# Optimization experiments

Measured on AMD Instinct MI355X. Metric: run time of the kernel, lower is better.

Reference implementation:

```python
import jax, jax.numpy as jnp
import numpy as np

B, N, D = 8, 1024, 256
H, DK, DV = 8, 64, 64
NEG = -1.0e9


def setup_inputs() -> dict:
    key = jax.random.key(0)
    ks = jax.random.split(key, 8)
    node_features = jax.random.normal(ks[0], (B, N, D), dtype=jnp.float32)
    em = (jax.random.uniform(ks[1], (B, 1, N, N)) < 0.03).astype(jnp.float32)
    eye = jnp.eye(N, dtype=jnp.float32)[None, None]
    edge_mask = jnp.maximum(em, eye)
    distance_weights = jax.random.uniform(ks[2], (B, N), dtype=jnp.float32)
    s = 1.0 / np.sqrt(D)
    Wq = jax.random.normal(ks[3], (D, H * DK), dtype=jnp.float32) * s
    Wk = jax.random.normal(ks[4], (D, H * DK), dtype=jnp.float32) * s
    Wv = jax.random.normal(ks[5], (D, H * DV), dtype=jnp.float32) * s
    Wo = jax.random.normal(ks[6], (H * DV, D), dtype=jnp.float32) / np.sqrt(H * DV)
    bo = jnp.zeros((D,), dtype=jnp.float32)
    return {"node_features": node_features, "edge_mask": edge_mask,
            "distance_weights": distance_weights,
            "Wq": Wq, "Wk": Wk, "Wv": Wv, "Wo": Wo, "bo": bo}


def reference(node_features, edge_mask, distance_weights, Wq, Wk, Wv, Wo, bo):
    b, n, d = node_features.shape
    # project and split heads: [B, H, N, dk]
    q = (node_features @ Wq).reshape(b, n, H, DK).transpose(0, 2, 1, 3)
    k = (node_features @ Wk).reshape(b, n, H, DK).transpose(0, 2, 1, 3)
    v = (node_features @ Wv).reshape(b, n, H, DV).transpose(0, 2, 1, 3)
    # scaled dot-product logits [B, H, N, N]
    logits = jnp.einsum('bhsd,bhtd->bhst', q, k) / jnp.sqrt(jnp.float32(DK))
    # additive edge-mask bias (masked pairs pushed to -1e9)
    logits = logits + (1.0 - edge_mask) * NEG
    # multiplicative per-key distance modulation
    logits = logits * distance_weights[:, None, None, :]
    w = jax.nn.softmax(logits, axis=-1)
    out = jnp.einsum('bhst,bhtd->bhsd', w, v)
    out = out.transpose(0, 2, 1, 3).reshape(b, n, H * DV)
    return out @ Wo + bo
```

## Files before the change

kernel.cpp:

```cpp
#include <hip/hip_runtime.h>
#include <hip/hip_bf16.h>
#include <hip/hip_fp16.h>
#include <cstdint>

#define B_ 8
#define N_ 1024
#define D_ 256
#define H_ 8
#define HD_ 512

typedef _Float16 f16;
typedef _Float16 f16x8 __attribute__((ext_vector_type(8)));
typedef _Float16 f16x4 __attribute__((ext_vector_type(4)));
typedef float f32x4 __attribute__((ext_vector_type(4)));
typedef unsigned long long ull;
typedef unsigned long long ull2 __attribute__((ext_vector_type(2)));

__device__ __forceinline__ void gload16(const void* g, void* l) {
    __builtin_amdgcn_global_load_lds(
        (const __attribute__((address_space(1))) unsigned int*)(uintptr_t)g,
        (__attribute__((address_space(3))) unsigned int*)(uintptr_t)l,
        16, 0, 0);
}

template<int RN>
__device__ __forceinline__ float rowror(float x) {
    return __builtin_bit_cast(float, __builtin_amdgcn_mov_dpp(
        __builtin_bit_cast(int, x), 0x120 + RN, 0xf, 0xf, true));
}
__device__ __forceinline__ float rowmax16(float x) {
    x = fmaxf(x, rowror<1>(x)); x = fmaxf(x, rowror<2>(x));
    x = fmaxf(x, rowror<4>(x)); x = fmaxf(x, rowror<8>(x));
    return x;
}
__device__ __forceinline__ float rowsum16(float x) {
    x += rowror<1>(x); x += rowror<2>(x);
    x += rowror<4>(x); x += rowror<8>(x);
    return x;
}

__global__ __launch_bounds__(256) void pack_mask_kernel(
    const float* __restrict__ mask, ull* __restrict__ bmT)
{
    const int wv = threadIdx.x >> 6, lane = threadIdx.x & 63;
    const int r = blockIdx.x * 4 + wv;
    const int b = r >> 10, n = r & 1023;
    const float* row = mask + ((size_t)b * N_ + n) * N_;
    for (int tt = 0; tt < 16; ++tt) {
        float v = row[tt * 64 + lane];
        ull m = __ballot(v != 0.0f);
        if (lane == 0) bmT[((size_t)b * 16 + tt) * N_ + n] = m;
    }
}

__global__ __launch_bounds__(256) void wconv_qkv_kernel(
    const float* __restrict__ Wq, const float* __restrict__ Wk,
    const float* __restrict__ Wv, f16* __restrict__ WT)
{
    __shared__ float Ws[64][65];
    const int tid = threadIdx.x;
    const int c0 = blockIdx.x * 64, k0 = blockIdx.y * 64;
    const int m = c0 >> 9, cw0 = c0 & 511;
    const float* Wsel = (m == 0) ? Wq : (m == 1) ? Wk : Wv;
    const float scale = (m == 0) ? 0.125f : 1.0f;
    const int rr = tid >> 6, cc = tid & 63;
    for (int i = 0; i < 16; ++i)
        Ws[i * 4 + rr][cc] = Wsel[(size_t)(k0 + i * 4 + rr) * HD_ + cw0 + cc];
    __syncthreads();
    for (int i = 0; i < 16; ++i)
        WT[(size_t)(c0 + i * 4 + rr) * D_ + k0 + cc] = (f16)(Ws[cc][i * 4 + rr] * scale);
}

__global__ __launch_bounds__(256) void wconv_o_kernel(
    const float* __restrict__ Wo, f16* __restrict__ WToT)
{
    __shared__ float Ws[64][65];
    const int tid = threadIdx.x;
    const int c0 = blockIdx.x * 64, k0 = blockIdx.y * 64;
    const int rr = tid >> 6, cc = tid & 63;
    for (int i = 0; i < 16; ++i)
        Ws[i * 4 + rr][cc] = Wo[(size_t)(k0 + i * 4 + rr) * D_ + c0 + cc];
    __syncthreads();
    for (int i = 0; i < 16; ++i)
        WToT[(size_t)(c0 + i * 4 + rr) * HD_ + k0 + cc] = (f16)Ws[cc][i * 4 + rr];
}

__global__ __launch_bounds__(256) void xconv_kernel(
    const float* __restrict__ X, f16* __restrict__ Xh)
{
    const size_t i = (size_t)(blockIdx.x * 256 + threadIdx.x) * 4;
    f32x4 v = *reinterpret_cast<const f32x4*>(X + i);
    f16x4 h;
    for (int j = 0; j < 4; ++j) h[j] = (f16)v[j];
    *reinterpret_cast<f16x4*>(Xh + i) = h;
}

__global__ __launch_bounds__(256, 4) void qkv_kernel(
    const f16* __restrict__ Xh, const f16* __restrict__ WT,
    f16* __restrict__ Qh, f16* __restrict__ Kh, f16* __restrict__ Vt)
{
    __shared__ f16 Wsh[2][8192];
    const int tid = threadIdx.x;
    const int wv = tid >> 6, lane = tid & 63;
    const int g = lane >> 4, li = lane & 15;
    const int row0 = blockIdx.x * 64;
    const int c0 = blockIdx.y * 128;
    const int m = c0 >> 9, cw0 = c0 & 511;

    f32x4 acc[4][2] = {};

    auto stage = [&](int ks, int bf) {
        for (int i = 0; i < 4; ++i) {
            const int idx = i * 256 + tid;
            const int c = idx >> 3, ch = idx & 7;
            const f16* src = WT + (size_t)(c0 + c) * D_ + ks * 64 + ((ch ^ (c & 7)) * 8);
            gload16(src, &Wsh[bf][idx * 8]);
        }
    };
    stage(0, 0);
    __syncthreads();
    int bf = 0;
    for (int ks = 0; ks < 4; ++ks) {
        if (ks < 3) stage(ks + 1, bf ^ 1);
        for (int kk = 0; kk < 2; ++kk) {
            f16x8 af[4];
            for (int rf = 0; rf < 4; ++rf)
                af[rf] = *reinterpret_cast<const f16x8*>(
                    Xh + (size_t)(row0 + rf * 16 + li) * D_ + ks * 64 + kk * 32 + g * 8);
            for (int cf = 0; cf < 2; ++cf) {
                const int cl = wv * 32 + cf * 16 + li;
                f16x8 bm_ = *reinterpret_cast<const f16x8*>(
                    &Wsh[bf][cl * 64 + (((kk * 4 + g) ^ (cl & 7)) * 8)]);
                for (int rf = 0; rf < 4; ++rf)
                    acc[rf][cf] = __builtin_amdgcn_mfma_f32_16x16x32_f16(
                        af[rf], bm_, acc[rf][cf], 0, 0, 0);
            }
        }
        __syncthreads();
        bf ^= 1;
    }
    const int b = row0 >> 10;
    for (int cf = 0; cf < 2; ++cf) {
        const int cw = cw0 + wv * 32 + cf * 16 + li;
        const int h = cw >> 6, dk = cw & 63;
        for (int rf = 0; rf < 4; ++rf) {
            const int nloc = (row0 & 1023) + rf * 16 + g * 4;
            if (m < 2) {
                f16* dst = (m == 0 ? Qh : Kh) + ((size_t)(b * H_ + h) * N_ + nloc) * 64 + dk;
                for (int j = 0; j < 4; ++j) dst[(size_t)j * 64] = (f16)acc[rf][cf][j];
            } else {
                f16x4 v4;
                for (int j = 0; j < 4; ++j) v4[j] = (f16)acc[rf][cf][j];
                *reinterpret_cast<f16x4*>(
                    Vt + ((size_t)(b * H_ + h) * 64 + dk) * N_ + nloc) = v4;
            }
        }
    }
}

__global__ __launch_bounds__(256, 4) void attn_kernel(
    const f16* __restrict__ Qh, const f16* __restrict__ Kh,
    const f16* __restrict__ Vt,
    const ull* __restrict__ bm, const float* __restrict__ dw,
    f16* __restrict__ AO)
{
    __shared__ f16 Ksh[8192];
    __shared__ f16 Vsh[8192];
    __shared__ f16 Ps[4096];
    const int tid = threadIdx.x;
    const int wv = tid >> 6, lane = tid & 63;
    const int g = lane >> 4, li = lane & 15;
    const int bid = (blockIdx.x & 7) * 128 + (blockIdx.x >> 3);
    const int st = bid & 15, h = (bid >> 4) & 7, b = bid >> 7;
    const int s0 = st * 64 + wv * 16;

    const f16* Qbase = Qh + (size_t)(b * H_ + h) * N_ * 64;
    const f16* Kbase = Kh + (size_t)(b * H_ + h) * N_ * 64;
    const f16* Vbase = Vt + (size_t)(b * H_ + h) * 64 * N_;

    f16x8 qf0 = *reinterpret_cast<const f16x8*>(Qbase + (size_t)(s0 + li) * 64 + g * 8);
    f16x8 qf1 = *reinterpret_cast<const f16x8*>(Qbase + (size_t)(s0 + li) * 64 + 32 + g * 8);

    int ro0[4], ro1[4];
    for (int fc = 0; fc < 4; ++fc) {
        const int r = fc * 16 + li;
        ro0[fc] = r * 64 + ((g ^ (r & 7)) * 8);
        ro1[fc] = r * 64 + (((4 | g) ^ (r & 7)) * 8);
    }
    const int pr0 = wv * 1024 + li * 64 + ((g ^ (li & 7)) * 8);
    const int pr1 = wv * 1024 + li * 64 + (((4 | g) ^ (li & 7)) * 8);

    const int s0i = wv * 64 + lane, s1i = 256 + wv * 64 + lane;
    const int r0_ = s0i >> 3, c0_ = ((s0i & 7) ^ (r0_ & 7)) * 8;
    const int r1_ = s1i >> 3, c1_ = ((s1i & 7) ^ (r1_ & 7)) * 8;
    const f16* kp0 = Kbase + r0_ * 64 + c0_;
    const f16* kp1 = Kbase + r1_ * 64 + c1_;
    const f16* vp0 = Vbase + (size_t)r0_ * N_ + c0_;
    const f16* vp1 = Vbase + (size_t)r1_ * N_ + c1_;
    f16* const kd0 = Ksh + s0i * 8;
    f16* const kd1 = Ksh + s1i * 8;
    f16* const vd0 = Vsh + s0i * 8;
    f16* const vd1 = Vsh + s1i * 8;

    const ull* bmp = bm + (size_t)b * 16 * N_ + s0 + g * 4;
    const float* dwp = dw + b * N_ + li;

    f32x4 of[4] = {};
    float m_run[4], l_run[4];
    for (int j = 0; j < 4; ++j) { m_run[j] = -1e30f; l_run[j] = 0.f; }

    gload16(kp0, kd0); gload16(kp1, kd1);
    gload16(vp0, vd0); gload16(vp1, vd1);
    kp0 += 4096; kp1 += 4096; vp0 += 64; vp1 += 64;
    __syncthreads();
    int koff = 0;

    for (int tt = 0; tt < 16; ++tt) {
        if (tt < 15) {
            const int nb = koff ^ 4096;
            gload16(kp0, kd0 + nb); gload16(kp1, kd1 + nb);
            gload16(vp0, vd0 + nb); gload16(vp1, vd1 + nb);
            kp0 += 4096; kp1 += 4096; vp0 += 64; vp1 += 64;
        }
        ull2 w01 = *reinterpret_cast<const ull2*>(bmp);
        ull2 w23 = *reinterpret_cast<const ull2*>(bmp + 2);
        bmp += N_;
        float dwc[4], bdw[4];
        for (int fc = 0; fc < 4; ++fc) {
            dwc[fc] = dwp[fc * 16] * 1.442695041f;
            bdw[fc] = dwc[fc] * -1.0e9f;
        }
        dwp += 64;

        f32x4 s[4] = {};
        for (int fc = 0; fc < 4; ++fc) {
            f16x8 kf0 = *reinterpret_cast<const f16x8*>(Ksh + koff + ro0[fc]);
            f16x8 kf1 = *reinterpret_cast<const f16x8*>(Ksh + koff + ro1[fc]);
            s[fc] = __builtin_amdgcn_mfma_f32_16x16x32_f16(qf0, kf0, s[fc], 0, 0, 0);
            s[fc] = __builtin_amdgcn_mfma_f32_16x16x32_f16(qf1, kf1, s[fc], 0, 0, 0);
        }
        ull wsh[4];
        wsh[0] = w01.x >> li; wsh[1] = w01.y >> li;
        wsh[2] = w23.x >> li; wsh[3] = w23.y >> li;

        float mt[4] = {-1e30f, -1e30f, -1e30f, -1e30f};
        for (int fc = 0; fc < 4; ++fc)
            for (int j = 0; j < 4; ++j) {
                const float sel = ((wsh[j] >> (fc * 16)) & 1ull) ? 0.0f : bdw[fc];
                const float lg = fmaf(s[fc][j], dwc[fc], sel);
                s[fc][j] = lg;
                mt[j] = fmaxf(mt[j], lg);
            }
        float alpha[4];
        for (int j = 0; j < 4; ++j) {
            mt[j] = rowmax16(mt[j]);
            const float mn = fmaxf(m_run[j], mt[j]);
            alpha[j] = __builtin_amdgcn_exp2f(m_run[j] - mn);
            m_run[j] = mn;
        }
        float rs[4] = {0.f, 0.f, 0.f, 0.f};
        for (int fc = 0; fc < 4; ++fc)
            for (int j = 0; j < 4; ++j) {
                const float p = __builtin_amdgcn_exp2f(s[fc][j] - m_run[j]);
                s[fc][j] = p;
                rs[j] += p;
            }
        for (int j = 0; j < 4; ++j) {
            rs[j] = rowsum16(rs[j]);
            l_run[j] = l_run[j] * alpha[j] + rs[j];
        }
        for (int fc = 0; fc < 4; ++fc)
            for (int j = 0; j < 4; ++j) of[fc][j] *= alpha[j];

        {
            f16* psw = Ps + wv * 1024;
            for (int fc = 0; fc < 4; ++fc)
                for (int j = 0; j < 4; ++j) {
                    const int r = g * 4 + j;
                    psw[r * 64 + (((fc * 2 + (li >> 3)) ^ (r & 7)) * 8) + (li & 7)]
                        = (f16)s[fc][j];
                }
            f16x8 pf0 = *reinterpret_cast<const f16x8*>(Ps + pr0);
            f16x8 pf1 = *reinterpret_cast<const f16x8*>(Ps + pr1);
            for (int fc = 0; fc < 4; ++fc) {
                f16x8 vf0 = *reinterpret_cast<const f16x8*>(Vsh + koff + ro0[fc]);
                f16x8 vf1 = *reinterpret_cast<const f16x8*>(Vsh + koff + ro1[fc]);
                of[fc] = __builtin_amdgcn_mfma_f32_16x16x32_f16(pf0, vf0, of[fc], 0, 0, 0);
                of[fc] = __builtin_amdgcn_mfma_f32_16x16x32_f16(pf1, vf1, of[fc], 0, 0, 0);
            }
        }
        __syncthreads();
        koff ^= 4096;
    }
    for (int j = 0; j < 4; ++j) {
        const float inv = 1.f / l_run[j];
        const int srow = s0 + g * 4 + j;
        f16* dst = AO + ((size_t)b * N_ + srow) * HD_ + h * 64;
        for (int fc = 0; fc < 4; ++fc)
            dst[fc * 16 + li] = (f16)(of[fc][j] * inv);
    }
}

__global__ __launch_bounds__(256, 4) void proj_kernel(
    const f16* __restrict__ AO, const f16* __restrict__ WToT,
    const float* __restrict__ bo, float* __restrict__ out)
{
    __shared__ f16 Ash[16 * 512];
    const int tid = threadIdx.x;
    const int wv = tid >> 6, lane = tid & 63;
    const int g = lane >> 4, li = lane & 15;
    const int row0 = blockIdx.x * 16;
    const int c0 = wv * 64;

    for (int i = 0; i < 4; ++i) {
        const int idx = i * 256 + tid;
        const int r = idx >> 6, ch = idx & 63;
        const f16* src = AO + (size_t)(row0 + r) * HD_ + ((ch ^ (r & 7)) * 8);
        gload16(src, &Ash[idx * 8]);
    }
    __syncthreads();

    f32x4 acc[4] = {};
    for (int k0 = 0; k0 < HD_; k0 += 32) {
        const int cb = k0 >> 3;
        f16x8 af = *reinterpret_cast<const f16x8*>(
            &Ash[li * HD_ + (((cb + g) ^ (li & 7)) * 8)]);
        for (int fc = 0; fc < 4; ++fc) {
            f16x8 bf = *reinterpret_cast<const f16x8*>(
                WToT + (size_t)(c0 + fc * 16 + li) * HD_ + k0 + g * 8);
            acc[fc] = __builtin_amdgcn_mfma_f32_16x16x32_f16(af, bf, acc[fc], 0, 0, 0);
        }
    }
    for (int fc = 0; fc < 4; ++fc) {
        const int c = c0 + fc * 16 + li;
        const float bias = bo[c];
        for (int j = 0; j < 4; ++j)
            out[(size_t)(row0 + g * 4 + j) * D_ + c] = acc[fc][j] + bias;
    }
}

extern "C" void kernel_launch(void* const* d_in, const int* in_sizes, int n_in,
                              void* d_out, int out_size, void* d_ws, size_t ws_size,
                              hipStream_t stream) {
    const float* X    = (const float*)d_in[0];
    const float* mask = (const float*)d_in[1];
    const float* dwv  = (const float*)d_in[2];
    const float* Wq   = (const float*)d_in[3];
    const float* Wk   = (const float*)d_in[4];
    const float* Wv   = (const float*)d_in[5];
    const float* Wo   = (const float*)d_in[6];
    const float* bo   = (const float*)d_in[7];
    float* out = (float*)d_out;

    const size_t per = (size_t)B_ * H_ * N_ * 64;
    f16* Qh = (f16*)d_ws;
    f16* Kh = Qh + per;
    f16* Vt = Kh + per;
    f16* AO = Vt + per;
    f16* WToT = (f16*)d_ws;

    ull* bmT   = (ull*)d_out;
    f16* WTqkv = (f16*)((char*)d_out + (1u << 20));
    f16* Xh    = (f16*)((char*)d_out + (2u << 20));

    pack_mask_kernel<<<dim3(2048), 256, 0, stream>>>(mask, bmT);
    wconv_qkv_kernel<<<dim3(24, 4), 256, 0, stream>>>(Wq, Wk, Wv, WTqkv);
    xconv_kernel<<<dim3(2048), 256, 0, stream>>>(X, Xh);
    qkv_kernel<<<dim3(128, 12), 256, 0, stream>>>(Xh, WTqkv, Qh, Kh, Vt);
    attn_kernel<<<dim3(1024), 256, 0, stream>>>(Qh, Kh, Vt, bmT, dwv, AO);
    wconv_o_kernel<<<dim3(4, 8), 256, 0, stream>>>(Wo, WToT);
    proj_kernel<<<dim3(512, 1), 256, 0, stream>>>(AO, WToT, bo, out);
}
```

Before: 198.7 us.

## Merge preprocessing kernels, stage X in LDS, lazy softmax rescale, MFMA priority

Three preprocessing launches (mask bit-packing, QKV weight transpose, X fp16 conversion) become one kernel that dispatches on block index, removing two launches. The QKV GEMM now stages X tiles into swizzled LDS with async global-to-LDS loads instead of reading fragments straight from global memory, and its occupancy hint drops from 4 to 3. The attention kernel skips the online-softmax rescale of the accumulator and running sum unless some row's max grows by more than 8 in log2 units. s_setprio brackets are added around MFMA sections. The lazy rescale lets exponentials exceed 1 and trades a wave-wide vote for skipped multiplies.

```diff
diff --git a/kernel.cpp b/kernel.cpp
--- a/kernel.cpp
+++ b/kernel.cpp
@@ -39,36 +39,45 @@
     return x;
 }
 
-__global__ __launch_bounds__(256) void pack_mask_kernel(
-    const float* __restrict__ mask, ull* __restrict__ bmT)
-{
-    const int wv = threadIdx.x >> 6, lane = threadIdx.x & 63;
-    const int r = blockIdx.x * 4 + wv;
-    const int b = r >> 10, n = r & 1023;
-    const float* row = mask + ((size_t)b * N_ + n) * N_;
-    for (int tt = 0; tt < 16; ++tt) {
-        float v = row[tt * 64 + lane];
-        ull m = __ballot(v != 0.0f);
-        if (lane == 0) bmT[((size_t)b * 16 + tt) * N_ + n] = m;
-    }
-}
-
-__global__ __launch_bounds__(256) void wconv_qkv_kernel(
+__global__ __launch_bounds__(256) void pre_kernel(
+    const float* __restrict__ mask, ull* __restrict__ bmT,
     const float* __restrict__ Wq, const float* __restrict__ Wk,
-    const float* __restrict__ Wv, f16* __restrict__ WT)
+    const float* __restrict__ Wv, f16* __restrict__ WT,
+    const float* __restrict__ X, f16* __restrict__ Xh)
 {
     __shared__ float Ws[64][65];
-    const int tid = threadIdx.x;
-    const int c0 = blockIdx.x * 64, k0 = blockIdx.y * 64;
-    const int m = c0 >> 9, cw0 = c0 & 511;
-    const float* Wsel = (m == 0) ? Wq : (m == 1) ? Wk : Wv;
-    const float scale = (m == 0) ? 0.125f : 1.0f;
-    const int rr = tid >> 6, cc = tid & 63;
-    for (int i = 0; i < 16; ++i)
-        Ws[i * 4 + rr][cc] = Wsel[(size_t)(k0 + i * 4 + rr) * HD_ + cw0 + cc];
-    __syncthreads();
-    for (int i = 0; i < 16; ++i)
-        WT[(size_t)(c0 + i * 4 + rr) * D_ + k0 + cc] = (f16)(Ws[cc][i * 4 + rr] * scale);
+    const int bid = blockIdx.x;
+    const int tid = threadIdx.x;
+    if (bid < 2048) {
+        const int wv = tid >> 6, lane = tid & 63;
+        const int r = bid * 4 + wv;
+        const int b = r >> 10, n = r & 1023;
+        const float* row = mask + ((size_t)b * N_ + n) * N_;
+        for (int tt = 0; tt < 16; ++tt) {
+            float v = row[tt * 64 + lane];
+            ull m = __ballot(v != 0.0f);
+            if (lane == 0) bmT[((size_t)b * 16 + tt) * N_ + n] = m;
+        }
+    } else if (bid < 2144) {
+        const int t = bid - 2048;
+        const int c0 = (t % 24) * 64, k0 = (t / 24) * 64;
+        const int m = c0 >> 9, cw0 = c0 & 511;
+        const float* Wsel = (m == 0) ? Wq : (m == 1) ? Wk : Wv;
+        const float scale = (m == 0) ? 0.125f : 1.0f;
+        const int rr = tid >> 6, cc = tid & 63;
+        for (int i = 0; i < 16; ++i)
+            Ws[i * 4 + rr][cc] = Wsel[(size_t)(k0 + i * 4 + rr) * HD_ + cw0 + cc];
+        __syncthreads();
+        for (int i = 0; i < 16; ++i)
+            WT[(size_t)(c0 + i * 4 + rr) * D_ + k0 + cc] =
+                (f16)(Ws[cc][i * 4 + rr] * scale);
+    } else {
+        const size_t i = (size_t)((bid - 2144) * 256 + tid) * 4;
+        f32x4 v = *reinterpret_cast<const f32x4*>(X + i);
+        f16x4 h2;
+        for (int j = 0; j < 4; ++j) h2[j] = (f16)v[j];
+        *reinterpret_cast<f16x4*>(Xh + i) = h2;
+    }
 }
 
 __global__ __launch_bounds__(256) void wconv_o_kernel(
@@ -85,20 +94,11 @@
         WToT[(size_t)(c0 + i * 4 + rr) * HD_ + k0 + cc] = (f16)Ws[cc][i * 4 + rr];
 }
 
-__global__ __launch_bounds__(256) void xconv_kernel(
-    const float* __restrict__ X, f16* __restrict__ Xh)
-{
-    const size_t i = (size_t)(blockIdx.x * 256 + threadIdx.x) * 4;
-    f32x4 v = *reinterpret_cast<const f32x4*>(X + i);
-    f16x4 h;
-    for (int j = 0; j < 4; ++j) h[j] = (f16)v[j];
-    *reinterpret_cast<f16x4*>(Xh + i) = h;
-}
-
-__global__ __launch_bounds__(256, 4) void qkv_kernel(
+__global__ __launch_bounds__(256, 3) void qkv_kernel(
     const f16* __restrict__ Xh, const f16* __restrict__ WT,
     f16* __restrict__ Qh, f16* __restrict__ Kh, f16* __restrict__ Vt)
 {
+    __shared__ f16 Ash[2][4096];
     __shared__ f16 Wsh[2][8192];
     const int tid = threadIdx.x;
     const int wv = tid >> 6, lane = tid & 63;
@@ -110,6 +110,12 @@
     f32x4 acc[4][2] = {};
 
     auto stage = [&](int ks, int bf) {
+        for (int i = 0; i < 2; ++i) {
+            const int idx = i * 256 + tid;
+            const int r = idx >> 3, ch = idx & 7;
+            const f16* src = Xh + (size_t)(row0 + r) * D_ + ks * 64 + ((ch ^ (r & 7)) * 8);
+            gload16(src, &Ash[bf][idx * 8]);
+        }
         for (int i = 0; i < 4; ++i) {
             const int idx = i * 256 + tid;
             const int c = idx >> 3, ch = idx & 7;
@@ -124,9 +130,12 @@
         if (ks < 3) stage(ks + 1, bf ^ 1);
         for (int kk = 0; kk < 2; ++kk) {
             f16x8 af[4];
-            for (int rf = 0; rf < 4; ++rf)
+            for (int rf = 0; rf < 4; ++rf) {
+                const int r = rf * 16 + li;
                 af[rf] = *reinterpret_cast<const f16x8*>(
-                    Xh + (size_t)(row0 + rf * 16 + li) * D_ + ks * 64 + kk * 32 + g * 8);
+                    &Ash[bf][r * 64 + (((kk * 4 + g) ^ (r & 7)) * 8)]);
+            }
+            __builtin_amdgcn_s_setprio(1);
             for (int cf = 0; cf < 2; ++cf) {
                 const int cl = wv * 32 + cf * 16 + li;
                 f16x8 bm_ = *reinterpret_cast<const f16x8*>(
@@ -135,6 +144,7 @@
                     acc[rf][cf] = __builtin_amdgcn_mfma_f32_16x16x32_f16(
                         af[rf], bm_, acc[rf][cf], 0, 0, 0);
             }
+            __builtin_amdgcn_s_setprio(0);
         }
         __syncthreads();
         bf ^= 1;
@@ -233,12 +243,15 @@
         dwp += 64;
 
         f32x4 s[4] = {};
+        __builtin_amdgcn_s_setprio(1);
         for (int fc = 0; fc < 4; ++fc) {
             f16x8 kf0 = *reinterpret_cast<const f16x8*>(Ksh + koff + ro0[fc]);
             f16x8 kf1 = *reinterpret_cast<const f16x8*>(Ksh + koff + ro1[fc]);
             s[fc] = __builtin_amdgcn_mfma_f32_16x16x32_f16(qf0, kf0, s[fc], 0, 0, 0);
             s[fc] = __builtin_amdgcn_mfma_f32_16x16x32_f16(qf1, kf1, s[fc], 0, 0, 0);
         }
+        __builtin_amdgcn_s_setprio(0);
+
         ull wsh[4];
         wsh[0] = w01.x >> li; wsh[1] = w01.y >> li;
         wsh[2] = w23.x >> li; wsh[3] = w23.y >> li;
@@ -251,12 +264,18 @@
                 s[fc][j] = lg;
                 mt[j] = fmaxf(mt[j], lg);
             }
-        float alpha[4];
-        for (int j = 0; j < 4; ++j) {
-            mt[j] = rowmax16(mt[j]);
-            const float mn = fmaxf(m_run[j], mt[j]);
-            alpha[j] = __builtin_amdgcn_exp2f(m_run[j] - mn);
-            m_run[j] = mn;
+        for (int j = 0; j < 4; ++j) mt[j] = rowmax16(mt[j]);
+
+        const bool small = (mt[0] - m_run[0] <= 8.f) & (mt[1] - m_run[1] <= 8.f) &
+                           (mt[2] - m_run[2] <= 8.f) & (mt[3] - m_run[3] <= 8.f);
+        if (!__all(small)) {
+            for (int j = 0; j < 4; ++j) {
+                const float mn = fmaxf(m_run[j], mt[j]);
+                const float alpha = __builtin_amdgcn_exp2f(m_run[j] - mn);
+                m_run[j] = mn;
+                l_run[j] *= alpha;
+                for (int fc = 0; fc < 4; ++fc) of[fc][j] *= alpha;
+            }
         }
         float rs[4] = {0.f, 0.f, 0.f, 0.f};
         for (int fc = 0; fc < 4; ++fc)
@@ -265,12 +284,8 @@
                 s[fc][j] = p;
                 rs[j] += p;
             }
-        for (int j = 0; j < 4; ++j) {
-            rs[j] = rowsum16(rs[j]);
-            l_run[j] = l_run[j] * alpha[j] + rs[j];
-        }
-        for (int fc = 0; fc < 4; ++fc)
-            for (int j = 0; j < 4; ++j) of[fc][j] *= alpha[j];
+        for (int j = 0; j < 4; ++j)
+            l_run[j] += rowsum16(rs[j]);
 
         {
             f16* psw = Ps + wv * 1024;
@@ -282,12 +297,14 @@
                 }
             f16x8 pf0 = *reinterpret_cast<const f16x8*>(Ps + pr0);
             f16x8 pf1 = *reinterpret_cast<const f16x8*>(Ps + pr1);
+            __builtin_amdgcn_s_setprio(1);
             for (int fc = 0; fc < 4; ++fc) {
                 f16x8 vf0 = *reinterpret_cast<const f16x8*>(Vsh + koff + ro0[fc]);
                 f16x8 vf1 = *reinterpret_cast<const f16x8*>(Vsh + koff + ro1[fc]);
                 of[fc] = __builtin_amdgcn_mfma_f32_16x16x32_f16(pf0, vf0, of[fc], 0, 0, 0);
                 of[fc] = __builtin_amdgcn_mfma_f32_16x16x32_f16(pf1, vf1, of[fc], 0, 0, 0);
             }
+            __builtin_amdgcn_s_setprio(0);
         }
         __syncthreads();
         koff ^= 4096;
@@ -363,9 +380,8 @@
     f16* WTqkv = (f16*)((char*)d_out + (1u << 20));
     f16* Xh    = (f16*)((char*)d_out + (2u << 20));
 
-    pack_mask_kernel<<<dim3(2048), 256, 0, stream>>>(mask, bmT);
-    wconv_qkv_kernel<<<dim3(24, 4), 256, 0, stream>>>(Wq, Wk, Wv, WTqkv);
-    xconv_kernel<<<dim3(2048), 256, 0, stream>>>(X, Xh);
+    pre_kernel<<<dim3(2048 + 96 + 2048), 256, 0, stream>>>(
+        mask, bmT, Wq, Wk, Wv, WTqkv, X, Xh);
     qkv_kernel<<<dim3(128, 12), 256, 0, stream>>>(Xh, WTqkv, Qh, Kh, Vt);
     attn_kernel<<<dim3(1024), 256, 0, stream>>>(Qh, Kh, Vt, bmT, dwv, AO);
     wconv_o_kernel<<<dim3(4, 8), 256, 0, stream>>>(Wo, WToT);
```

Result: faster. 172.7 us (-13.1%).
